# Kernel tuning notes

Hardware: AMD Instinct MI355X
Metric: run time of the kernel (lower is better)

The kernel has to match this reference:

```python
import jax, jax.numpy as jnp
import numpy as np

N = 500_000
D_IN, D_HID, NUM_HEADS, D_OUT = 256, 128, 4, 4


def setup_inputs() -> dict:
    key = jax.random.key(0)
    k1, k2, k3, k4 = jax.random.split(key, 4)
    x = jax.random.normal(k1, (N, D_IN), dtype=jnp.float32)
    W1 = jax.random.normal(k2, (D_IN, D_HID), dtype=jnp.float32)
    W2 = jax.random.normal(k3, (D_HID, D_OUT), dtype=jnp.float32)
    heads = jax.random.randint(k4, (N,), 0, NUM_HEADS, dtype=jnp.int32)
    return {"x": x, "W1": W1, "W2": W2, "heads": heads}


def reference(x, W1, W2, heads):
    # linear_1: e3nn Linear over pure-scalar irreps == dense matmul with
    # path normalization 1/sqrt(fan_in)
    h = (x @ W1) * (1.0 / np.sqrt(D_IN))          # [N, D_HID]
    # gated nonlinearity (scalars only -> plain activation)
    h = jax.nn.silu(h)
    # mask_head: channels grouped into NUM_HEADS blocks of D_HID//NUM_HEADS;
    # keep only the block matching each node's head
    hb = h.reshape(N, NUM_HEADS, D_HID // NUM_HEADS)
    onehot = jax.nn.one_hot(heads, NUM_HEADS, dtype=h.dtype)  # [N, H]
    h = (hb * onehot[:, :, None]).reshape(N, D_HID)
    # linear_2
    return (h @ W2) * (1.0 / np.sqrt(D_HID))      # [N, D_OUT]
```

## Files before the change

### kernel.cpp

```cpp
#include <hip/hip_runtime.h>
#include <hip/hip_bf16.h>


#define D_IN   256
#define TILE_M 128

typedef __attribute__((ext_vector_type(8))) short  short8;
typedef __attribute__((ext_vector_type(4))) float  float4v;
typedef __attribute__((ext_vector_type(4))) int    int4v;

__device__ __forceinline__ unsigned short f2bf_rne(float f) {
    union { float f; unsigned int u; } cv; cv.f = f;
    unsigned int u = cv.u;
    return (unsigned short)((u + 0x7FFFu + ((u >> 16) & 1u)) >> 16);
}

__device__ __forceinline__ short8 pack8(float4v lo, float4v hi) {
    short8 r;
    r[0] = (short)__bfloat16_as_ushort(__float2bfloat16(lo[0]));
    r[1] = (short)__bfloat16_as_ushort(__float2bfloat16(lo[1]));
    r[2] = (short)__bfloat16_as_ushort(__float2bfloat16(lo[2]));
    r[3] = (short)__bfloat16_as_ushort(__float2bfloat16(lo[3]));
    r[4] = (short)__bfloat16_as_ushort(__float2bfloat16(hi[0]));
    r[5] = (short)__bfloat16_as_ushort(__float2bfloat16(hi[1]));
    r[6] = (short)__bfloat16_as_ushort(__float2bfloat16(hi[2]));
    r[7] = (short)__bfloat16_as_ushort(__float2bfloat16(hi[3]));
    return r;
}

__global__ void prep_w1(const float* __restrict__ W1, unsigned short* __restrict__ W1p) {
    int idx = blockIdx.x * 256 + threadIdx.x;
    int i = idx >> 7;
    int j = idx & 127;
    unsigned short b = f2bf_rne(W1[idx] * 0.0625f);
    int kt = i >> 5, q = (i >> 3) & 3, jj = i & 7;
    int nt = j >> 4, mm = j & 15;
    int lane = q * 16 + mm;
    W1p[(((kt * 8 + nt) * 64 + lane) << 3) + jj] = b;
}

__global__ __launch_bounds__(256)
void readout_v4(const float* __restrict__ x,
                const unsigned short* __restrict__ W1p,
                const float* __restrict__ W2,
                const int* __restrict__ heads,
                float* __restrict__ out, int nrows) {
    __shared__ unsigned short sB[16384];

    const int t    = threadIdx.x;
    const int w    = t >> 6;
    const int lane = t & 63;
    const int q    = lane >> 4;
    const int m    = lane & 15;
    const int rowbase = blockIdx.x * TILE_M + w * 32;

    const int r0 = min(rowbase + m,      nrows - 1);
    const int r1 = min(rowbase + 16 + m, nrows - 1);
    const float* xr0 = x + (size_t)r0 * D_IN + q * 8;
    const float* xr1 = x + (size_t)r1 * D_IN + q * 8;
    const unsigned short* sbase = sB + lane * 8;

    float4v acc[2][8];
    #pragma unroll
    for (int rt = 0; rt < 2; ++rt)
        #pragma unroll
        for (int nt = 0; nt < 8; ++nt) acc[rt][nt] = (float4v){0.f, 0.f, 0.f, 0.f};

    #pragma unroll
    for (int p = 0; p < 2; ++p) {
        if (p) __syncthreads();
        {
            const unsigned short* gsrc = W1p + p * 16384 + t * 8;
            float4v v[8];
            #pragma unroll
            for (int i = 0; i < 8; ++i)
                v[i] = *(const float4v*)(gsrc + i * 2048);
            #pragma unroll
            for (int i = 0; i < 8; ++i)
                *(float4v*)(sB + t * 8 + i * 2048) = v[i];
        }
        __syncthreads();

        #pragma unroll
        for (int ktl = 0; ktl < 4; ++ktl) {
            const int kt = p * 4 + ktl;
            float4v a0lo = *(const float4v*)(xr0 + kt * 32);
            float4v a0hi = *(const float4v*)(xr0 + kt * 32 + 4);
            float4v a1lo = *(const float4v*)(xr1 + kt * 32);
            float4v a1hi = *(const float4v*)(xr1 + kt * 32 + 4);
            short8 b[8];
            #pragma unroll
            for (int nt = 0; nt < 8; ++nt)
                b[nt] = *(const short8*)(sbase + (ktl * 8 + nt) * 512);
            short8 a0 = pack8(a0lo, a0hi);
            short8 a1 = pack8(a1lo, a1hi);
            #pragma unroll
            for (int nt = 0; nt < 8; ++nt) {
                acc[0][nt] = __builtin_amdgcn_mfma_f32_16x16x32_bf16(a0, b[nt], acc[0][nt], 0, 0, 0);
                acc[1][nt] = __builtin_amdgcn_mfma_f32_16x16x32_bf16(a1, b[nt], acc[1][nt], 0, 0, 0);
            }
        }
    }

    const float sc = 0.08838834764831845f;
    const bool full = (rowbase + 32) <= nrows;
    #pragma unroll
    for (int rt = 0; rt < 2; ++rt) {
        int4v hv;
        if (full) {
            hv = *(const int4v*)(heads + rowbase + rt * 16 + q * 4);
        } else {
            #pragma unroll
            for (int e = 0; e < 4; ++e)
                hv[e] = heads[min(rowbase + rt * 16 + q * 4 + e, nrows - 1)];
        }
        #pragma unroll
        for (int reg = 0; reg < 4; ++reg) {
            int h = hv[reg];
            float v0 = (h == 0) ? acc[rt][0][reg] : (h == 1) ? acc[rt][2][reg]
                     : (h == 2) ? acc[rt][4][reg] : acc[rt][6][reg];
            float v1 = (h == 0) ? acc[rt][1][reg] : (h == 1) ? acc[rt][3][reg]
                     : (h == 2) ? acc[rt][5][reg] : acc[rt][7][reg];
            float s0 = v0 / (1.0f + __expf(-v0));
            float s1 = v1 / (1.0f + __expf(-v1));
            float4v w2a = *(const float4v*)(W2 + (h * 32 + m) * 4);
            float4v w2b = *(const float4v*)(W2 + (h * 32 + 16 + m) * 4);
            float4v o = w2a * s0 + w2b * s1;
            #pragma unroll
            for (int d = 1; d < 16; d <<= 1) {
                o[0] += __shfl_xor(o[0], d, 64);
                o[1] += __shfl_xor(o[1], d, 64);
                o[2] += __shfl_xor(o[2], d, 64);
                o[3] += __shfl_xor(o[3], d, 64);
            }
            if (m == 0) {
                int gr = rowbase + rt * 16 + q * 4 + reg;
                if (gr < nrows) {
                    float4v res = { o[0] * sc, o[1] * sc, o[2] * sc, o[3] * sc };
                    *(float4v*)(out + (size_t)gr * 4) = res;
                }
            }
        }
    }
}

extern "C" void kernel_launch(void* const* d_in, const int* in_sizes, int n_in,
                              void* d_out, int out_size, void* d_ws, size_t ws_size,
                              hipStream_t stream) {
    const float* x     = (const float*)d_in[0];
    const float* W1    = (const float*)d_in[1];
    const float* W2    = (const float*)d_in[2];
    const int*   heads = (const int*)d_in[3];
    float*       out   = (float*)d_out;
    unsigned short* W1p = (unsigned short*)d_ws;

    int nrows = in_sizes[0] / D_IN;

    prep_w1<<<128, 256, 0, stream>>>(W1, W1p);
    int nb = (nrows + TILE_M - 1) / TILE_M;
    readout_v4<<<nb, 256, 0, stream>>>(x, W1p, W2, heads, out, nrows);
}
```

Baseline: 686.9 us.

## Make readout kernel persistent with full W1 resident in shared memory

The kernel becomes a grid-stride persistent kernel with 512 blocks. Each block loads all of W1 (64 KB bf16) into LDS once, then loops over row tiles, which removes the per-tile reload of W1 and the mid-loop barrier. In exchange, LDS use per block doubles, which caps occupancy at about two blocks per CU. Each wave also issues its x loads without other blocks' memory traffic overlapping the W1 staging, which may hurt latency hiding on a stream that is bound by x bandwidth.

New measurement: 761.2 us. +10.8%, slower.

```diff
diff --git a/kernel.cpp b/kernel.cpp
--- a/kernel.cpp
+++ b/kernel.cpp
@@ -39,51 +39,50 @@
     W1p[(((kt * 8 + nt) * 64 + lane) << 3) + jj] = b;
 }
 
-__global__ __launch_bounds__(256)
-void readout_v4(const float* __restrict__ x,
+__global__ __launch_bounds__(256, 2)
+void readout_v5(const float* __restrict__ x,
                 const unsigned short* __restrict__ W1p,
                 const float* __restrict__ W2,
                 const int* __restrict__ heads,
                 float* __restrict__ out, int nrows) {
-    __shared__ unsigned short sB[16384];
+    __shared__ unsigned short sB[32768];
 
     const int t    = threadIdx.x;
     const int w    = t >> 6;
     const int lane = t & 63;
     const int q    = lane >> 4;
     const int m    = lane & 15;
-    const int rowbase = blockIdx.x * TILE_M + w * 32;
 
-    const int r0 = min(rowbase + m,      nrows - 1);
-    const int r1 = min(rowbase + 16 + m, nrows - 1);
-    const float* xr0 = x + (size_t)r0 * D_IN + q * 8;
-    const float* xr1 = x + (size_t)r1 * D_IN + q * 8;
+    {
+        const unsigned short* gsrc = W1p + t * 8;
+        #pragma unroll
+        for (int i = 0; i < 16; ++i) {
+            float4v v = *(const float4v*)(gsrc + i * 2048);
+            *(float4v*)(sB + t * 8 + i * 2048) = v;
+        }
+    }
+    __syncthreads();
+
     const unsigned short* sbase = sB + lane * 8;
+    const float sc = 0.08838834764831845f;
+    const int ntiles = (nrows + TILE_M - 1) / TILE_M;
 
-    float4v acc[2][8];
-    #pragma unroll
-    for (int rt = 0; rt < 2; ++rt)
+    for (int tile = blockIdx.x; tile < ntiles; tile += gridDim.x) {
+        const int rowbase = tile * TILE_M + w * 32;
+
+        const int r0 = min(rowbase + m,      nrows - 1);
+        const int r1 = min(rowbase + 16 + m, nrows - 1);
+        const float* xr0 = x + (size_t)r0 * D_IN + q * 8;
+        const float* xr1 = x + (size_t)r1 * D_IN + q * 8;
+
+        float4v acc[2][8];
         #pragma unroll
-        for (int nt = 0; nt < 8; ++nt) acc[rt][nt] = (float4v){0.f, 0.f, 0.f, 0.f};
-
-    #pragma unroll
-    for (int p = 0; p < 2; ++p) {
-        if (p) __syncthreads();
-        {
-            const unsigned short* gsrc = W1p + p * 16384 + t * 8;
-            float4v v[8];
+        for (int rt = 0; rt < 2; ++rt)
             #pragma unroll
-            for (int i = 0; i < 8; ++i)
-                v[i] = *(const float4v*)(gsrc + i * 2048);
-            #pragma unroll
-            for (int i = 0; i < 8; ++i)
-                *(float4v*)(sB + t * 8 + i * 2048) = v[i];
-        }
-        __syncthreads();
+            for (int nt = 0; nt < 8; ++nt) acc[rt][nt] = (float4v){0.f, 0.f, 0.f, 0.f};
 
         #pragma unroll
-        for (int ktl = 0; ktl < 4; ++ktl) {
-            const int kt = p * 4 + ktl;
+        for (int kt = 0; kt < 8; ++kt) {
             float4v a0lo = *(const float4v*)(xr0 + kt * 32);
             float4v a0hi = *(const float4v*)(xr0 + kt * 32 + 4);
             float4v a1lo = *(const float4v*)(xr1 + kt * 32);
@@ -91,7 +90,7 @@
             short8 b[8];
             #pragma unroll
             for (int nt = 0; nt < 8; ++nt)
-                b[nt] = *(const short8*)(sbase + (ktl * 8 + nt) * 512);
+                b[nt] = *(const short8*)(sbase + (kt * 8 + nt) * 512);
             short8 a0 = pack8(a0lo, a0hi);
             short8 a1 = pack8(a1lo, a1hi);
             #pragma unroll
@@ -100,44 +99,43 @@
                 acc[1][nt] = __builtin_amdgcn_mfma_f32_16x16x32_bf16(a1, b[nt], acc[1][nt], 0, 0, 0);
             }
         }
-    }
 
-    const float sc = 0.08838834764831845f;
-    const bool full = (rowbase + 32) <= nrows;
-    #pragma unroll
-    for (int rt = 0; rt < 2; ++rt) {
-        int4v hv;
-        if (full) {
-            hv = *(const int4v*)(heads + rowbase + rt * 16 + q * 4);
-        } else {
+        const bool full = (rowbase + 32) <= nrows;
+        #pragma unroll
+        for (int rt = 0; rt < 2; ++rt) {
+            int4v hv;
+            if (full) {
+                hv = *(const int4v*)(heads + rowbase + rt * 16 + q * 4);
+            } else {
+                #pragma unroll
+                for (int e = 0; e < 4; ++e)
+                    hv[e] = heads[min(rowbase + rt * 16 + q * 4 + e, nrows - 1)];
+            }
             #pragma unroll
-            for (int e = 0; e < 4; ++e)
-                hv[e] = heads[min(rowbase + rt * 16 + q * 4 + e, nrows - 1)];
-        }
-        #pragma unroll
-        for (int reg = 0; reg < 4; ++reg) {
-            int h = hv[reg];
-            float v0 = (h == 0) ? acc[rt][0][reg] : (h == 1) ? acc[rt][2][reg]
-                     : (h == 2) ? acc[rt][4][reg] : acc[rt][6][reg];
-            float v1 = (h == 0) ? acc[rt][1][reg] : (h == 1) ? acc[rt][3][reg]
-                     : (h == 2) ? acc[rt][5][reg] : acc[rt][7][reg];
-            float s0 = v0 / (1.0f + __expf(-v0));
-            float s1 = v1 / (1.0f + __expf(-v1));
-            float4v w2a = *(const float4v*)(W2 + (h * 32 + m) * 4);
-            float4v w2b = *(const float4v*)(W2 + (h * 32 + 16 + m) * 4);
-            float4v o = w2a * s0 + w2b * s1;
-            #pragma unroll
-            for (int d = 1; d < 16; d <<= 1) {
-                o[0] += __shfl_xor(o[0], d, 64);
-                o[1] += __shfl_xor(o[1], d, 64);
-                o[2] += __shfl_xor(o[2], d, 64);
-                o[3] += __shfl_xor(o[3], d, 64);
-            }
-            if (m == 0) {
-                int gr = rowbase + rt * 16 + q * 4 + reg;
-                if (gr < nrows) {
-                    float4v res = { o[0] * sc, o[1] * sc, o[2] * sc, o[3] * sc };
-                    *(float4v*)(out + (size_t)gr * 4) = res;
+            for (int reg = 0; reg < 4; ++reg) {
+                int h = hv[reg];
+                float v0 = (h == 0) ? acc[rt][0][reg] : (h == 1) ? acc[rt][2][reg]
+                         : (h == 2) ? acc[rt][4][reg] : acc[rt][6][reg];
+                float v1 = (h == 0) ? acc[rt][1][reg] : (h == 1) ? acc[rt][3][reg]
+                         : (h == 2) ? acc[rt][5][reg] : acc[rt][7][reg];
+                float s0 = v0 / (1.0f + __expf(-v0));
+                float s1 = v1 / (1.0f + __expf(-v1));
+                float4v w2a = *(const float4v*)(W2 + (h * 32 + m) * 4);
+                float4v w2b = *(const float4v*)(W2 + (h * 32 + 16 + m) * 4);
+                float4v o = w2a * s0 + w2b * s1;
+                #pragma unroll
+                for (int d = 1; d < 16; d <<= 1) {
+                    o[0] += __shfl_xor(o[0], d, 64);
+                    o[1] += __shfl_xor(o[1], d, 64);
+                    o[2] += __shfl_xor(o[2], d, 64);
+                    o[3] += __shfl_xor(o[3], d, 64);
+                }
+                if (m == 0) {
+                    int gr = rowbase + rt * 16 + q * 4 + reg;
+                    if (gr < nrows) {
+                        float4v res = { o[0] * sc, o[1] * sc, o[2] * sc, o[3] * sc };
+                        *(float4v*)(out + (size_t)gr * 4) = res;
+                    }
                 }
             }
         }
@@ -157,6 +155,7 @@
     int nrows = in_sizes[0] / D_IN;
 
     prep_w1<<<128, 256, 0, stream>>>(W1, W1p);
-    int nb = (nrows + TILE_M - 1) / TILE_M;
-    readout_v4<<<nb, 256, 0, stream>>>(x, W1p, W2, heads, out, nrows);
+    int ntiles = (nrows + TILE_M - 1) / TILE_M;
+    int nb = min(512, ntiles);
+    readout_v5<<<nb, 256, 0, stream>>>(x, W1p, W2, heads, out, nrows);
 }
```
